# Kernel tuning notes

Measured on AMD Instinct MI355X. Metric: run time of the kernel, lower is better.

Reference implementation:

```python
import jax, jax.numpy as jnp
import numpy as np

B, L = 32, 100
NQ = 500
S = NQ + 1          # n_question + 1 skills
DK, DA, DE = 64, 64, 128
NE, NAT, NIT = 20000, 3000, 3000


def _xavier(k, shape):
    fan_out, fan_in = shape[0], shape[1]
    bound = float(np.sqrt(6.0 / (fan_in + fan_out)))
    return jax.random.uniform(k, shape, jnp.float32, -bound, bound)


def setup_inputs() -> dict:
    key = jax.random.key(0)
    ks = jax.random.split(key, 24)
    inp = {
        'e_data': jax.random.randint(ks[0], (B, L), 0, NE),
        'a_data': jax.random.randint(ks[1], (B, L), 0, 2, dtype=jnp.int32),
        'at_data': jax.random.randint(ks[2], (B, L), 0, NAT),
        'it_data': jax.random.randint(ks[3], (B, L), 0, NIT),
        'q_matrix': (jax.random.uniform(ks[4], (NE + 10, S)) < 0.05).astype(jnp.float32),
        'h0': _xavier(ks[5], (S, DK)),
        'e_embed': _xavier(ks[6], (NE + 10, DE)),
        'at_embed': _xavier(ks[7], (NAT + 10, DK)),
        'it_embed': _xavier(ks[8], (NIT + 10, DK)),
        'W1': _xavier(ks[9], (DK, DA + DE + DK)), 'b1': jnp.zeros((DK,)),
        'W2': _xavier(ks[10], (DK, 4 * DK)),      'b2': jnp.zeros((DK,)),
        'W3': _xavier(ks[11], (DK, 4 * DK)),      'b3': jnp.zeros((DK,)),
        'W4': _xavier(ks[12], (DK, 3 * DK)),      'b4': jnp.zeros((DK,)),
        'W5': _xavier(ks[13], (DK, DE + DK)),     'b5': jnp.zeros((DK,)),
    }
    return inp


def reference(e_data, a_data, at_data, it_data, q_matrix, h0, e_embed,
              at_embed, it_embed, W1, b1, W2, b2, W3, b3, W4, b4, W5, b5):
    b, l = e_data.shape
    dk = h0.shape[1]
    e_emb = e_embed[e_data]            # (B,L,DE)
    it_emb = it_embed[it_data]         # (B,L,DK)
    at_emb = at_embed[at_data]         # (B,L,DK)
    a_rep = jnp.broadcast_to(a_data.astype(jnp.float32)[:, :, None], (b, l, DA))
    # linear_1 over concat(e, at, a): all learning vectors, computed once
    all_learning = jnp.concatenate([e_emb, at_emb, a_rep], axis=2) @ W1.T + b1  # (B,L,DK)

    h_pre0 = jnp.broadcast_to(h0[None], (b,) + h0.shape)      # (B,S,DK)
    h_tilde0 = q_matrix[e_data[:, 0]] @ h0                    # (B,DK)
    learning0 = jnp.zeros((b, dk), jnp.float32)

    xs = dict(
        e_t=e_data[:, :-1].T,                                  # (L-1,B)
        it_t=jnp.swapaxes(it_emb[:, :-1], 0, 1),               # (L-1,B,DK)
        learn_t=jnp.swapaxes(all_learning[:, :-1], 0, 1),      # (L-1,B,DK)
        e_next=e_data[:, 1:].T,                                # (L-1,B)
        e_emb_next=jnp.swapaxes(e_emb[:, 1:], 0, 1),           # (L-1,B,DE)
    )

    def step(carry, x):
        h_pre, h_tilde_pre, learning_pre = carry
        q_e = q_matrix[x['e_t']]                               # (B,S)
        g_in = jnp.concatenate([learning_pre, x['it_t'], x['learn_t'], h_tilde_pre], 1)
        learning_gain = jnp.tanh(g_in @ W2.T + b2)
        gamma_l = jax.nn.sigmoid(g_in @ W3.T + b3)
        LG = gamma_l * (learning_gain + 1.0) * 0.5             # (B,DK)
        LG_tilde = q_e[:, :, None] * LG[:, None, :]            # (B,S,DK)
        s = h_pre.shape[1]
        f_in = jnp.concatenate([
            h_pre,
            jnp.broadcast_to(LG[:, None, :], (b, s, dk)),
            jnp.broadcast_to(x['it_t'][:, None, :], (b, s, dk)),
        ], axis=2)
        gamma_f = jax.nn.sigmoid(f_in @ W4.T + b4)             # (B,S,DK)
        h = LG_tilde + gamma_f * h_pre
        q_next = q_matrix[x['e_next']]                         # (B,S)
        h_tilde = jnp.einsum('bs,bsd->bd', q_next, h)
        y = jax.nn.sigmoid(jnp.concatenate([x['e_emb_next'], h_tilde], 1) @ W5.T + b5).sum(1) / dk
        return (h, h_tilde, x['learn_t']), y

    _, ys = jax.lax.scan(step, (h_pre0, h_tilde0, learning0), xs)
    pred = jnp.concatenate([jnp.zeros((b, 1), jnp.float32), ys.T], axis=1)  # (B,L)
    return pred
```

## Files before the change

kernel.cpp:

```cpp
#include <hip/hip_runtime.h>
#include <hip/hip_bf16.h>

namespace {

constexpr int B  = 32;
constexpr int L  = 100;
constexpr int S  = 501;
constexpr int DK = 64;
constexpr int DE = 128;

typedef __attribute__((ext_vector_type(8))) short short8v;
typedef __attribute__((ext_vector_type(4))) float f32x4;
typedef unsigned int u32;

__device__ __forceinline__ float sigm(float x) {
    return __fdividef(1.0f, 1.0f + __expf(-x));
}
__device__ __forceinline__ unsigned short f2bf(float f) {
    u32 u = __float_as_uint(f);
    u += 0x7FFFu + ((u >> 16) & 1u);
    return (unsigned short)(u >> 16);
}

__global__ __launch_bounds__(256) void k_init(
    const float* __restrict__ W1, const float* __restrict__ W2,
    const float* __restrict__ W3, const float* __restrict__ W4,
    const float* __restrict__ W5,
    float* __restrict__ W1T, float* __restrict__ W2T, float* __restrict__ W3T,
    float* __restrict__ W4T, float* __restrict__ W5T,
    float* __restrict__ pred)
{
    const int idx = blockIdx.x * 256 + threadIdx.x;
    const int st  = gridDim.x * 256;
    for (int i = idx; i < 64 * 256; i += st) {
        int dd = i >> 8, kk = i & 255;
        W1T[kk * 64 + dd] = W1[i];
        W2T[kk * 64 + dd] = W2[i];
        W3T[kk * 64 + dd] = W3[i];
    }
    for (int i = idx; i < 64 * 192; i += st) {
        int dd = i / 192, kk = i % 192;
        W4T[kk * 64 + dd] = W4[i];
        W5T[kk * 64 + dd] = W5[i];
    }
    if (idx < B) pred[idx * L] = 0.0f;
}

__global__ __launch_bounds__(256) void k_all_learning(
    const int* __restrict__ e_data, const int* __restrict__ a_data,
    const int* __restrict__ at_data,
    const float* __restrict__ e_embed, const float* __restrict__ at_embed,
    const float* __restrict__ W1T, const float* __restrict__ b1,
    float* __restrict__ allL)
{
    __shared__ float in_s[4][257];
    const int g = threadIdx.x >> 6;
    const int d = threadIdx.x & 63;
    const int row = blockIdx.x * 4 + g;
    const int e  = e_data[row];
    const int at = at_data[row];
    in_s[g][d]       = e_embed[(size_t)e * DE + d];
    in_s[g][64 + d]  = e_embed[(size_t)e * DE + 64 + d];
    in_s[g][128 + d] = at_embed[(size_t)at * DK + d];
    in_s[g][192 + d] = (float)a_data[row];
    __syncthreads();
    float acc = b1[d];
    #pragma unroll 8
    for (int k = 0; k < 256; ++k) acc += W1T[k * 64 + d] * in_s[g][k];
    allL[row * DK + d] = acc;
}

__global__ __launch_bounds__(256) void k_pre(
    const int* __restrict__ e_data, const int* __restrict__ it_data,
    const float* __restrict__ e_embed, const float* __restrict__ it_embed,
    const float* __restrict__ allL,
    const float* __restrict__ W2T, const float* __restrict__ W3T,
    const float* __restrict__ W4T, const float* __restrict__ W5T,
    const float* __restrict__ b2, const float* __restrict__ b3,
    const float* __restrict__ b4, const float* __restrict__ b5,
    float* __restrict__ G2, float* __restrict__ G3,
    float* __restrict__ G4it, float* __restrict__ prey)
{
    __shared__ float lp[4][64], its[4][64], ln[4][64], ee[4][128];
    const int g = threadIdx.x >> 6;
    const int d = threadIdx.x & 63;
    const int row = blockIdx.x * 4 + g;
    const int t = row % L;
    lp[g][d]  = (t == 0) ? 0.0f : allL[(row - 1) * 64 + d];
    its[g][d] = it_embed[(size_t)it_data[row] * 64 + d];
    ln[g][d]  = allL[row * 64 + d];
    const int e = e_data[row];
    ee[g][d]      = e_embed[(size_t)e * DE + d];
    ee[g][64 + d] = e_embed[(size_t)e * DE + 64 + d];
    __syncthreads();
    float g2 = b2[d], g3 = b3[d], g4 = b4[d], py = b5[d];
    #pragma unroll 4
    for (int k = 0; k < 64; ++k) {
        const float l0 = lp[g][k], i0 = its[g][k], n0 = ln[g][k];
        g2 += W2T[k * 64 + d] * l0 + W2T[(64 + k) * 64 + d] * i0 + W2T[(128 + k) * 64 + d] * n0;
        g3 += W3T[k * 64 + d] * l0 + W3T[(64 + k) * 64 + d] * i0 + W3T[(128 + k) * 64 + d] * n0;
        g4 += W4T[(128 + k) * 64 + d] * i0;
        py += W5T[k * 64 + d] * ee[g][k] + W5T[(64 + k) * 64 + d] * ee[g][64 + k];
    }
    G2[row * 64 + d]   = g2;
    G3[row * 64 + d]   = g3;
    G4it[row * 64 + d] = g4;
    prey[row * 64 + d] = py;
}

__global__ __launch_bounds__(512) void k_steps(
    const float* __restrict__ G2, const float* __restrict__ G3,
    const float* __restrict__ G4it,
    const float* __restrict__ W2, const float* __restrict__ W3,
    const float* __restrict__ W4,
    const float* __restrict__ q_matrix, const int* __restrict__ e_data,
    const float* __restrict__ h0, float* __restrict__ hthist)
{
    __shared__ unsigned short hB[512 * 72];
    __shared__ float qQ[2][512];
    __shared__ float htS[64], LGs[64], Vs[64];
    __shared__ float red[512], red2[512];
    __shared__ int eRow[128];

    const int tid = threadIdx.x;
    const int b   = blockIdx.x;
    const int l   = tid & 63;
    const int w   = tid >> 6;
    const int lm  = l & 15;
    const int lk  = l >> 4;
    const int d   = tid & 63;
    const int kg  = tid >> 6;

    float w2r[8], w3r[8], wbr[8];
    #pragma unroll
    for (int j = 0; j < 8; ++j) {
        w2r[j] = W2[d * 256 + 192 + kg * 8 + j];
        w3r[j] = W3[d * 256 + 192 + kg * 8 + j];
        wbr[j] = W4[d * 192 + 64  + kg * 8 + j];
    }

    short8v afr[4][2];
    #pragma unroll
    for (int dt = 0; dt < 4; ++dt)
        #pragma unroll
        for (int kc = 0; kc < 2; ++kc) {
            const float* src = W4 + (size_t)(dt * 16 + lm) * 192 + kc * 32 + lk * 8;
            union { unsigned short us[8]; short8v v; } u;
            #pragma unroll
            for (int j = 0; j < 8; ++j) u.us[j] = f2bf(src[j]);
            afr[dt][kc] = u.v;
        }

    if (tid < L) eRow[tid] = e_data[b * L + tid];

    f32x4 hreg[4][4];
    #pragma unroll
    for (int st = 0; st < 4; ++st) {
        const int s = (w * 4 + st) * 16 + lm;
        #pragma unroll
        for (int dt = 0; dt < 4; ++dt) {
            const int d0 = dt * 16 + lk * 4;
            f32x4 hv = {0.f, 0.f, 0.f, 0.f};
            if (s < S) hv = *(const f32x4*)(h0 + (size_t)s * 64 + d0);
            hreg[st][dt] = hv;
            const u32 lo = (u32)f2bf(hv.x) | ((u32)f2bf(hv.y) << 16);
            const u32 hi = (u32)f2bf(hv.z) | ((u32)f2bf(hv.w) << 16);
            *(uint2*)&hB[s * 72 + d0] = make_uint2(lo, hi);
        }
    }
    __syncthreads();
    qQ[0][tid] = (tid < S) ? q_matrix[(size_t)eRow[0] * S + tid] : 0.f;
    __syncthreads();

    {
        f32x4 part[4];
        #pragma unroll
        for (int dt = 0; dt < 4; ++dt) part[dt] = f32x4{0.f, 0.f, 0.f, 0.f};
        #pragma unroll
        for (int st = 0; st < 4; ++st) {
            const int s = (w * 4 + st) * 16 + lm;
            const float qe = qQ[0][s];
            #pragma unroll
            for (int dt = 0; dt < 4; ++dt) part[dt] += qe * hreg[st][dt];
        }
        #pragma unroll
        for (int dt = 0; dt < 4; ++dt)
            #pragma unroll
            for (int i = 0; i < 4; ++i) {
                float v = part[dt][i];
                v += __shfl_xor(v, 1); v += __shfl_xor(v, 2);
                v += __shfl_xor(v, 4); v += __shfl_xor(v, 8);
                part[dt][i] = v;
            }
        if (lm == 0) {
            #pragma unroll
            for (int dt = 0; dt < 4; ++dt)
                *(f32x4*)&red[w * 64 + dt * 16 + lk * 4] = part[dt];
        }
        __syncthreads();
        if (tid < 64) {
            float sm = 0.f;
            #pragma unroll
            for (int ww = 0; ww < 8; ++ww) sm += red[ww * 64 + tid];
            htS[tid] = sm;
        }
        __syncthreads();
    }

    for (int t = 0; t < L - 1; ++t) {
        const int cur = t & 1, nxt = cur ^ 1;

        short8v bfr[4][2];
        #pragma unroll
        for (int st = 0; st < 4; ++st) {
            const int s = (w * 4 + st) * 16 + lm;
            #pragma unroll
            for (int kc = 0; kc < 2; ++kc)
                bfr[st][kc] = *(const short8v*)&hB[s * 72 + kc * 32 + lk * 8];
        }

        const float qn = (tid < S) ? q_matrix[(size_t)eRow[t + 1] * S + tid] : 0.f;
        float g2v = 0.f, g3v = 0.f, g4v = 0.f;
        if (tid < 64) {
            g2v = G2[(b * L + t) * 64 + d];
            g3v = G3[(b * L + t) * 64 + d];
            g4v = G4it[(b * L + t) * 64 + d];
        }

        {
            float p2 = 0.f, p3 = 0.f;
            #pragma unroll
            for (int j = 0; j < 8; ++j) {
                const float hv = htS[kg * 8 + j];
                p2 += w2r[j] * hv;
                p3 += w3r[j] * hv;
            }
            red[kg * 64 + d] = p2;
            red2[kg * 64 + d] = p3;
        }
        qQ[nxt][tid] = qn;
        __syncthreads();
        if (tid < 64) {
            float g2 = g2v, g3 = g3v;
            #pragma unroll
            for (int ww = 0; ww < 8; ++ww) { g2 += red[ww * 64 + d]; g3 += red2[ww * 64 + d]; }
            LGs[d] = sigm(g3) * (tanhf(g2) + 1.0f) * 0.5f;
        }
        __syncthreads();
        {
            float pv = 0.f;
            #pragma unroll
            for (int j = 0; j < 8; ++j) pv += wbr[j] * LGs[kg * 8 + j];
            red[kg * 64 + d] = pv;
        }
        __syncthreads();
        if (tid < 64) {
            float v = g4v;
            #pragma unroll
            for (int ww = 0; ww < 8; ++ww) v += red[ww * 64 + d];
            Vs[d] = v;
        }
        __syncthreads();

        f32x4 part[4];
        #pragma unroll
        for (int dt = 0; dt < 4; ++dt) part[dt] = f32x4{0.f, 0.f, 0.f, 0.f};

        #pragma unroll
        for (int half = 0; half < 2; ++half) {
            f32x4 acc[2][4];
            #pragma unroll
            for (int d2 = 0; d2 < 2; ++d2)
                #pragma unroll
                for (int st = 0; st < 4; ++st) acc[d2][st] = f32x4{0.f, 0.f, 0.f, 0.f};

            #pragma unroll
            for (int d2 = 0; d2 < 2; ++d2) {
                const int dt = half * 2 + d2;
                #pragma unroll
                for (int st = 0; st < 4; ++st) {
                    acc[d2][st] = __builtin_amdgcn_mfma_f32_16x16x32_bf16(
                        afr[dt][0], bfr[st][0], acc[d2][st], 0, 0, 0);
                    acc[d2][st] = __builtin_amdgcn_mfma_f32_16x16x32_bf16(
                        afr[dt][1], bfr[st][1], acc[d2][st], 0, 0, 0);
                }
            }

            #pragma unroll
            for (int d2 = 0; d2 < 2; ++d2) {
                const int dt = half * 2 + d2;
                const int d0 = dt * 16 + lk * 4;
                const f32x4 lg4 = *(const f32x4*)&LGs[d0];
                const f32x4 v4  = *(const f32x4*)&Vs[d0];
                #pragma unroll
                for (int st = 0; st < 4; ++st) {
                    const int s = (w * 4 + st) * 16 + lm;
                    const float qe = qQ[cur][s];
                    const float qq = qQ[nxt][s];
                    const f32x4 a  = acc[d2][st];
                    const f32x4 ho = hreg[st][dt];
                    f32x4 hn;
                    hn.x = qe * lg4.x + sigm(a.x + v4.x) * ho.x;
                    hn.y = qe * lg4.y + sigm(a.y + v4.y) * ho.y;
                    hn.z = qe * lg4.z + sigm(a.z + v4.z) * ho.z;
                    hn.w = qe * lg4.w + sigm(a.w + v4.w) * ho.w;
                    hreg[st][dt] = hn;
                    const u32 lo = (u32)f2bf(hn.x) | ((u32)f2bf(hn.y) << 16);
                    const u32 hi = (u32)f2bf(hn.z) | ((u32)f2bf(hn.w) << 16);
                    *(uint2*)&hB[s * 72 + d0] = make_uint2(lo, hi);
                    part[dt] += qq * hn;
                }
            }
        }

        #pragma unroll
        for (int dt = 0; dt < 4; ++dt)
            #pragma unroll
            for (int i = 0; i < 4; ++i) {
                float v = part[dt][i];
                v += __shfl_xor(v, 1); v += __shfl_xor(v, 2);
                v += __shfl_xor(v, 4); v += __shfl_xor(v, 8);
                part[dt][i] = v;
            }
        if (lm == 0) {
            #pragma unroll
            for (int dt = 0; dt < 4; ++dt)
                *(f32x4*)&red[w * 64 + dt * 16 + lk * 4] = part[dt];
        }
        __syncthreads();
        if (tid < 64) {
            float sm = 0.f;
            #pragma unroll
            for (int ww = 0; ww < 8; ++ww) sm += red[ww * 64 + tid];
            htS[tid] = sm;
            hthist[(size_t)(t + 1) * (B * 64) + b * 64 + tid] = sm;
        }
        __syncthreads();
    }
}

__global__ __launch_bounds__(64) void k_y(
    const float* __restrict__ hthist, const float* __restrict__ prey,
    const float* __restrict__ W5T, float* __restrict__ pred)
{
    __shared__ float HT[64];
    const int j = blockIdx.x + 1;
    const int b = blockIdx.y;
    const int d = threadIdx.x;
    HT[d] = hthist[(size_t)j * (B * 64) + b * 64 + d];
    __syncthreads();
    float acc = prey[(b * L + j) * 64 + d];
    #pragma unroll 8
    for (int k = 0; k < 64; ++k) acc += W5T[(128 + k) * 64 + d] * HT[k];
    float y = sigm(acc);
    #pragma unroll
    for (int m = 1; m < 64; m <<= 1) y += __shfl_xor(y, m);
    if (d == 0) pred[b * L + j] = y * (1.0f / 64.0f);
}

}

extern "C" void kernel_launch(void* const* d_in, const int* in_sizes, int n_in,
                              void* d_out, int out_size, void* d_ws, size_t ws_size,
                              hipStream_t stream)
{
    const int*   e_data   = (const int*)d_in[0];
    const int*   a_data   = (const int*)d_in[1];
    const int*   at_data  = (const int*)d_in[2];
    const int*   it_data  = (const int*)d_in[3];
    const float* q_matrix = (const float*)d_in[4];
    const float* h0       = (const float*)d_in[5];
    const float* e_embed  = (const float*)d_in[6];
    const float* at_embed = (const float*)d_in[7];
    const float* it_embed = (const float*)d_in[8];
    const float* W1 = (const float*)d_in[9];  const float* b1 = (const float*)d_in[10];
    const float* W2 = (const float*)d_in[11]; const float* b2 = (const float*)d_in[12];
    const float* W3 = (const float*)d_in[13]; const float* b3 = (const float*)d_in[14];
    const float* W4 = (const float*)d_in[15]; const float* b4 = (const float*)d_in[16];
    const float* W5 = (const float*)d_in[17]; const float* b5 = (const float*)d_in[18];
    float* pred = (float*)d_out;

    float* ws   = (float*)d_ws;
    float* W1T    = ws;
    float* W2T    = W1T    + 16384;
    float* W3T    = W2T    + 16384;
    float* W4T    = W3T    + 16384;
    float* W5T    = W4T    + 12288;
    float* allL   = W5T    + 12288;
    float* G2     = allL   + 204800;
    float* G3     = G2     + 204800;
    float* G4it   = G3     + 204800;
    float* prey   = G4it   + 204800;
    float* hthist = prey   + 204800;

    hipLaunchKernelGGL(k_init, dim3(64), dim3(256), 0, stream,
                       W1, W2, W3, W4, W5, W1T, W2T, W3T, W4T, W5T, pred);
    hipLaunchKernelGGL(k_all_learning, dim3(B * L / 4), dim3(256), 0, stream,
                       e_data, a_data, at_data, e_embed, at_embed, W1T, b1, allL);
    hipLaunchKernelGGL(k_pre, dim3(B * L / 4), dim3(256), 0, stream,
                       e_data, it_data, e_embed, it_embed, allL,
                       W2T, W3T, W4T, W5T, b2, b3, b4, b5, G2, G3, G4it, prey);
    hipLaunchKernelGGL(k_steps, dim3(B), dim3(512), 0, stream,
                       G2, G3, G4it, W2, W3, W4, q_matrix, e_data, h0, hthist);
    hipLaunchKernelGGL(k_y, dim3(L - 1, B), dim3(64), 0, stream,
                       hthist, prey, W5T, pred);
}
```

Before: 798.8 us.

## Collapse per-step gate matvecs into one wave to cut block barriers

The per-step W2/W3/W4 gate matvecs, previously split across all 8 waves with shared-memory reductions and four barriers, are now computed by a single wave. That wave reads weights staged in LDS, which removes three __syncthreads per timestep. The q_matrix row and the G2/G3/G4 values are prefetched one step ahead into registers, and the h_tilde history is buffered in LDS and written to global memory once at the end. In exchange, the matvec work is serialized on 64 threads and LDS use grows to roughly 150KB.

```diff
diff --git a/kernel.cpp b/kernel.cpp
--- a/kernel.cpp
+++ b/kernel.cpp
@@ -108,19 +108,22 @@
     prey[row * 64 + d] = py;
 }
 
-__global__ __launch_bounds__(512) void k_steps(
+__global__ __launch_bounds__(512, 1) void k_steps(
     const float* __restrict__ G2, const float* __restrict__ G3,
     const float* __restrict__ G4it,
-    const float* __restrict__ W2, const float* __restrict__ W3,
-    const float* __restrict__ W4,
+    const float* __restrict__ W2T, const float* __restrict__ W3T,
+    const float* __restrict__ W4T, const float* __restrict__ W4,
     const float* __restrict__ q_matrix, const int* __restrict__ e_data,
     const float* __restrict__ h0, float* __restrict__ hthist)
 {
     __shared__ unsigned short hB[512 * 72];
     __shared__ float qQ[2][512];
-    __shared__ float htS[64], LGs[64], Vs[64];
-    __shared__ float red[512], red2[512];
-    __shared__ int eRow[128];
+    __shared__ float2 w23S[64 * 64];
+    __shared__ float  w4bS[64 * 64];
+    __shared__ float  htH[100 * 64];
+    __shared__ float  LGs[64], Vs[64], htS[64];
+    __shared__ float  red[8 * 64];
+    __shared__ int    eRow[104];
 
     const int tid = threadIdx.x;
     const int b   = blockIdx.x;
@@ -128,16 +131,13 @@
     const int w   = tid >> 6;
     const int lm  = l & 15;
     const int lk  = l >> 4;
-    const int d   = tid & 63;
-    const int kg  = tid >> 6;
-
-    float w2r[8], w3r[8], wbr[8];
-    #pragma unroll
-    for (int j = 0; j < 8; ++j) {
-        w2r[j] = W2[d * 256 + 192 + kg * 8 + j];
-        w3r[j] = W3[d * 256 + 192 + kg * 8 + j];
-        wbr[j] = W4[d * 192 + 64  + kg * 8 + j];
-    }
+
+    for (int i = tid; i < 4096; i += 512) {
+        const int k = i >> 6, dd = i & 63;
+        w23S[i] = make_float2(W2T[(192 + k) * 64 + dd], W3T[(192 + k) * 64 + dd]);
+        w4bS[i] = W4T[(64 + k) * 64 + dd];
+    }
+    if (tid < L) eRow[tid] = e_data[b * L + tid];
 
     short8v afr[4][2];
     #pragma unroll
@@ -150,8 +150,6 @@
             for (int j = 0; j < 8; ++j) u.us[j] = f2bf(src[j]);
             afr[dt][kc] = u.v;
         }
-
-    if (tid < L) eRow[tid] = e_data[b * L + tid];
 
     f32x4 hreg[4][4];
     #pragma unroll
@@ -169,7 +167,19 @@
         }
     }
     __syncthreads();
-    qQ[0][tid] = (tid < S) ? q_matrix[(size_t)eRow[0] * S + tid] : 0.f;
+
+    float qn_reg;
+    {
+        const float q0 = (tid < S) ? q_matrix[(size_t)eRow[0] * S + tid] : 0.f;
+        qQ[0][tid] = q0;
+        qn_reg = (tid < S) ? q_matrix[(size_t)eRow[1] * S + tid] : 0.f;
+    }
+    float g2v = 0.f, g3v = 0.f, g4v = 0.f;
+    if (tid < 64) {
+        g2v = G2[(b * L) * 64 + l];
+        g3v = G3[(b * L) * 64 + l];
+        g4v = G4it[(b * L) * 64 + l];
+    }
     __syncthreads();
 
     {
@@ -197,19 +207,17 @@
             for (int dt = 0; dt < 4; ++dt)
                 *(f32x4*)&red[w * 64 + dt * 16 + lk * 4] = part[dt];
         }
-        __syncthreads();
-        if (tid < 64) {
-            float sm = 0.f;
-            #pragma unroll
-            for (int ww = 0; ww < 8; ++ww) sm += red[ww * 64 + tid];
-            htS[tid] = sm;
-        }
-        __syncthreads();
-    }
+    }
+    __syncthreads();
 
     for (int t = 0; t < L - 1; ++t) {
         const int cur = t & 1, nxt = cur ^ 1;
 
+        qQ[nxt][tid] = qn_reg;
+        {
+            const int tn = (t + 2 < L) ? t + 2 : L - 1;
+            qn_reg = (tid < S) ? q_matrix[(size_t)eRow[tn] * S + tid] : 0.f;
+        }
         short8v bfr[4][2];
         #pragma unroll
         for (int st = 0; st < 4; ++st) {
@@ -219,46 +227,39 @@
                 bfr[st][kc] = *(const short8v*)&hB[s * 72 + kc * 32 + lk * 8];
         }
 
-        const float qn = (tid < S) ? q_matrix[(size_t)eRow[t + 1] * S + tid] : 0.f;
-        float g2v = 0.f, g3v = 0.f, g4v = 0.f;
         if (tid < 64) {
-            g2v = G2[(b * L + t) * 64 + d];
-            g3v = G3[(b * L + t) * 64 + d];
-            g4v = G4it[(b * L + t) * 64 + d];
-        }
-
-        {
-            float p2 = 0.f, p3 = 0.f;
-            #pragma unroll
-            for (int j = 0; j < 8; ++j) {
-                const float hv = htS[kg * 8 + j];
-                p2 += w2r[j] * hv;
-                p3 += w3r[j] * hv;
-            }
-            red[kg * 64 + d] = p2;
-            red2[kg * 64 + d] = p3;
-        }
-        qQ[nxt][tid] = qn;
-        __syncthreads();
-        if (tid < 64) {
-            float g2 = g2v, g3 = g3v;
-            #pragma unroll
-            for (int ww = 0; ww < 8; ++ww) { g2 += red[ww * 64 + d]; g3 += red2[ww * 64 + d]; }
-            LGs[d] = sigm(g3) * (tanhf(g2) + 1.0f) * 0.5f;
-        }
-        __syncthreads();
-        {
-            float pv = 0.f;
-            #pragma unroll
-            for (int j = 0; j < 8; ++j) pv += wbr[j] * LGs[kg * 8 + j];
-            red[kg * 64 + d] = pv;
-        }
-        __syncthreads();
-        if (tid < 64) {
-            float v = g4v;
-            #pragma unroll
-            for (int ww = 0; ww < 8; ++ww) v += red[ww * 64 + d];
-            Vs[d] = v;
+            const float g2c = g2v, g3c = g3v, g4c = g4v;
+            g2v = G2[(b * L + t + 1) * 64 + l];
+            g3v = G3[(b * L + t + 1) * 64 + l];
+            g4v = G4it[(b * L + t + 1) * 64 + l];
+
+            float htd = 0.f;
+            #pragma unroll
+            for (int ww = 0; ww < 8; ++ww) htd += red[ww * 64 + l];
+            htS[l] = htd;
+            htH[t * 64 + l] = htd;
+
+            float g2 = g2c, g3 = g3c;
+            #pragma unroll
+            for (int k4 = 0; k4 < 16; ++k4) {
+                const f32x4 h4 = *(const f32x4*)&htS[k4 * 4];
+                #pragma unroll
+                for (int j = 0; j < 4; ++j) {
+                    const float2 wv = w23S[(k4 * 4 + j) * 64 + l];
+                    g2 += wv.x * h4[j];
+                    g3 += wv.y * h4[j];
+                }
+            }
+            const float lg = sigm(g3) * (tanhf(g2) + 1.0f) * 0.5f;
+            LGs[l] = lg;
+            float v = g4c;
+            #pragma unroll
+            for (int k4 = 0; k4 < 16; ++k4) {
+                const f32x4 lg4 = *(const f32x4*)&LGs[k4 * 4];
+                #pragma unroll
+                for (int j = 0; j < 4; ++j) v += w4bS[(k4 * 4 + j) * 64 + l] * lg4[j];
+            }
+            Vs[l] = v;
         }
         __syncthreads();
 
@@ -328,15 +329,17 @@
                 *(f32x4*)&red[w * 64 + dt * 16 + lk * 4] = part[dt];
         }
         __syncthreads();
-        if (tid < 64) {
-            float sm = 0.f;
-            #pragma unroll
-            for (int ww = 0; ww < 8; ++ww) sm += red[ww * 64 + tid];
-            htS[tid] = sm;
-            hthist[(size_t)(t + 1) * (B * 64) + b * 64 + tid] = sm;
-        }
-        __syncthreads();
-    }
+    }
+
+    if (tid < 64) {
+        float htd = 0.f;
+        #pragma unroll
+        for (int ww = 0; ww < 8; ++ww) htd += red[ww * 64 + l];
+        htH[99 * 64 + l] = htd;
+    }
+    __syncthreads();
+    for (int i = tid; i < 100 * 64; i += 512)
+        hthist[(size_t)(i >> 6) * (B * 64) + b * 64 + (i & 63)] = htH[i];
 }
 
 __global__ __launch_bounds__(64) void k_y(
@@ -401,7 +404,8 @@
                        e_data, it_data, e_embed, it_embed, allL,
                        W2T, W3T, W4T, W5T, b2, b3, b4, b5, G2, G3, G4it, prey);
     hipLaunchKernelGGL(k_steps, dim3(B), dim3(512), 0, stream,
-                       G2, G3, G4it, W2, W3, W4, q_matrix, e_data, h0, hthist);
+                       G2, G3, G4it, W2T, W3T, W4T, W4,
+                       q_matrix, e_data, h0, hthist);
     hipLaunchKernelGGL(k_y, dim3(L - 1, B), dim3(64), 0, stream,
                        hthist, prey, W5T, pred);
 }
```

Result: slower. 1.360 ms (+70.3%).

## Prefetch q rows and G inputs a step ahead and shorten ht reductions

Applied to the files above, without the earlier changes.

The recurrent step kernel now loads the q_matrix row two steps ahead into a register and packs the current and next q values into one float2 shared array. It also loads next-step G2/G3/G4 values early, so global latency is hidden behind the current step. The h_tilde reduction uses two shuffle stages plus a 32-way shared-memory sum instead of four shuffles, and the h_tilde history is staged in LDS and written out once at the end. This raises LDS use (about 25KB more) and sets launch bounds to one block per SM.

```diff
diff --git a/kernel.cpp b/kernel.cpp
--- a/kernel.cpp
+++ b/kernel.cpp
@@ -20,6 +20,9 @@
     u32 u = __float_as_uint(f);
     u += 0x7FFFu + ((u >> 16) & 1u);
     return (unsigned short)(u >> 16);
+}
+__device__ __forceinline__ u32 pack2(float a, float b) {
+    return (u32)f2bf(a) | ((u32)f2bf(b) << 16);
 }
 
 __global__ __launch_bounds__(256) void k_init(
@@ -108,7 +111,7 @@
     prey[row * 64 + d] = py;
 }
 
-__global__ __launch_bounds__(512) void k_steps(
+__global__ __launch_bounds__(512, 1) void k_steps(
     const float* __restrict__ G2, const float* __restrict__ G3,
     const float* __restrict__ G4it,
     const float* __restrict__ W2, const float* __restrict__ W3,
@@ -117,10 +120,12 @@
     const float* __restrict__ h0, float* __restrict__ hthist)
 {
     __shared__ unsigned short hB[512 * 72];
-    __shared__ float qQ[2][512];
+    __shared__ float2 qP[512];
+    __shared__ float htH[100 * 64];
     __shared__ float htS[64], LGs[64], Vs[64];
     __shared__ float red[512], red2[512];
-    __shared__ int eRow[128];
+    __shared__ float red4[32 * 64];
+    __shared__ int eRow[104];
 
     const int tid = threadIdx.x;
     const int b   = blockIdx.x;
@@ -163,13 +168,23 @@
             f32x4 hv = {0.f, 0.f, 0.f, 0.f};
             if (s < S) hv = *(const f32x4*)(h0 + (size_t)s * 64 + d0);
             hreg[st][dt] = hv;
-            const u32 lo = (u32)f2bf(hv.x) | ((u32)f2bf(hv.y) << 16);
-            const u32 hi = (u32)f2bf(hv.z) | ((u32)f2bf(hv.w) << 16);
-            *(uint2*)&hB[s * 72 + d0] = make_uint2(lo, hi);
-        }
-    }
-    __syncthreads();
-    qQ[0][tid] = (tid < S) ? q_matrix[(size_t)eRow[0] * S + tid] : 0.f;
+            *(uint2*)&hB[s * 72 + d0] =
+                make_uint2(pack2(hv.x, hv.y), pack2(hv.z, hv.w));
+        }
+    }
+    __syncthreads();
+
+    {
+        const float q0 = (tid < S) ? q_matrix[(size_t)eRow[0] * S + tid] : 0.f;
+        const float q1 = (tid < S) ? q_matrix[(size_t)eRow[1] * S + tid] : 0.f;
+        qP[tid] = make_float2(q0, q1);
+    }
+    float g2v = 0.f, g3v = 0.f, g4v = 0.f;
+    if (tid < 64) {
+        g2v = G2[(b * L) * 64 + l];
+        g3v = G3[(b * L) * 64 + l];
+        g4v = G4it[(b * L) * 64 + l];
+    }
     __syncthreads();
 
     {
@@ -179,7 +194,7 @@
         #pragma unroll
         for (int st = 0; st < 4; ++st) {
             const int s = (w * 4 + st) * 16 + lm;
-            const float qe = qQ[0][s];
+            const float qe = qP[s].x;
             #pragma unroll
             for (int dt = 0; dt < 4; ++dt) part[dt] += qe * hreg[st][dt];
         }
@@ -189,27 +204,36 @@
             for (int i = 0; i < 4; ++i) {
                 float v = part[dt][i];
                 v += __shfl_xor(v, 1); v += __shfl_xor(v, 2);
-                v += __shfl_xor(v, 4); v += __shfl_xor(v, 8);
                 part[dt][i] = v;
             }
-        if (lm == 0) {
+        if ((lm & 3) == 0) {
+            const int g = w * 4 + (lm >> 2);
             #pragma unroll
             for (int dt = 0; dt < 4; ++dt)
-                *(f32x4*)&red[w * 64 + dt * 16 + lk * 4] = part[dt];
-        }
-        __syncthreads();
-        if (tid < 64) {
-            float sm = 0.f;
-            #pragma unroll
-            for (int ww = 0; ww < 8; ++ww) sm += red[ww * 64 + tid];
-            htS[tid] = sm;
-        }
-        __syncthreads();
-    }
+                *(f32x4*)&red4[g * 64 + dt * 16 + lk * 4] = part[dt];
+        }
+    }
+    __syncthreads();
+    if (tid < 64) {
+        float htd = 0.f;
+        #pragma unroll
+        for (int g = 0; g < 32; ++g) htd += red4[g * 64 + l];
+        htS[l] = htd;
+        htH[l] = htd;
+    }
+    __syncthreads();
+
+    float qn_reg = 0.f;
 
     for (int t = 0; t < L - 1; ++t) {
-        const int cur = t & 1, nxt = cur ^ 1;
-
+        if (t > 0) {
+            const float2 qold = qP[tid];
+            qP[tid] = make_float2(qold.y, qn_reg);
+        }
+        {
+            const int tn = (t + 2 < L) ? t + 2 : L - 1;
+            qn_reg = (tid < S) ? q_matrix[(size_t)eRow[tn] * S + tid] : 0.f;
+        }
         short8v bfr[4][2];
         #pragma unroll
         for (int st = 0; st < 4; ++st) {
@@ -218,28 +242,20 @@
             for (int kc = 0; kc < 2; ++kc)
                 bfr[st][kc] = *(const short8v*)&hB[s * 72 + kc * 32 + lk * 8];
         }
-
-        const float qn = (tid < S) ? q_matrix[(size_t)eRow[t + 1] * S + tid] : 0.f;
-        float g2v = 0.f, g3v = 0.f, g4v = 0.f;
-        if (tid < 64) {
-            g2v = G2[(b * L + t) * 64 + d];
-            g3v = G3[(b * L + t) * 64 + d];
-            g4v = G4it[(b * L + t) * 64 + d];
-        }
-
         {
+            const f32x4 h4a = *(const f32x4*)&htS[kg * 8];
+            const f32x4 h4b = *(const f32x4*)&htS[kg * 8 + 4];
             float p2 = 0.f, p3 = 0.f;
             #pragma unroll
-            for (int j = 0; j < 8; ++j) {
-                const float hv = htS[kg * 8 + j];
-                p2 += w2r[j] * hv;
-                p3 += w3r[j] * hv;
+            for (int j = 0; j < 4; ++j) {
+                p2 += w2r[j] * h4a[j] + w2r[4 + j] * h4b[j];
+                p3 += w3r[j] * h4a[j] + w3r[4 + j] * h4b[j];
             }
-            red[kg * 64 + d] = p2;
+            red[kg * 64 + d]  = p2;
             red2[kg * 64 + d] = p3;
         }
-        qQ[nxt][tid] = qn;
-        __syncthreads();
+        __syncthreads();
+
         if (tid < 64) {
             float g2 = g2v, g3 = g3v;
             #pragma unroll
@@ -247,20 +263,32 @@
             LGs[d] = sigm(g3) * (tanhf(g2) + 1.0f) * 0.5f;
         }
         __syncthreads();
+
         {
+            const f32x4 l4a = *(const f32x4*)&LGs[kg * 8];
+            const f32x4 l4b = *(const f32x4*)&LGs[kg * 8 + 4];
             float pv = 0.f;
             #pragma unroll
-            for (int j = 0; j < 8; ++j) pv += wbr[j] * LGs[kg * 8 + j];
+            for (int j = 0; j < 4; ++j)
+                pv += wbr[j] * l4a[j] + wbr[4 + j] * l4b[j];
             red[kg * 64 + d] = pv;
         }
         __syncthreads();
+
         if (tid < 64) {
             float v = g4v;
             #pragma unroll
             for (int ww = 0; ww < 8; ++ww) v += red[ww * 64 + d];
             Vs[d] = v;
-        }
-        __syncthreads();
+            g2v = G2[(b * L + t + 1) * 64 + l];
+            g3v = G3[(b * L + t + 1) * 64 + l];
+            g4v = G4it[(b * L + t + 1) * 64 + l];
+        }
+        __syncthreads();
+
+        float2 qv[4];
+        #pragma unroll
+        for (int st = 0; st < 4; ++st) qv[st] = qP[(w * 4 + st) * 16 + lm];
 
         f32x4 part[4];
         #pragma unroll
@@ -295,8 +323,8 @@
                 #pragma unroll
                 for (int st = 0; st < 4; ++st) {
                     const int s = (w * 4 + st) * 16 + lm;
-                    const float qe = qQ[cur][s];
-                    const float qq = qQ[nxt][s];
+                    const float qe = qv[st].x;
+                    const float qq = qv[st].y;
                     const f32x4 a  = acc[d2][st];
                     const f32x4 ho = hreg[st][dt];
                     f32x4 hn;
@@ -305,9 +333,8 @@
                     hn.z = qe * lg4.z + sigm(a.z + v4.z) * ho.z;
                     hn.w = qe * lg4.w + sigm(a.w + v4.w) * ho.w;
                     hreg[st][dt] = hn;
-                    const u32 lo = (u32)f2bf(hn.x) | ((u32)f2bf(hn.y) << 16);
-                    const u32 hi = (u32)f2bf(hn.z) | ((u32)f2bf(hn.w) << 16);
-                    *(uint2*)&hB[s * 72 + d0] = make_uint2(lo, hi);
+                    *(uint2*)&hB[s * 72 + d0] =
+                        make_uint2(pack2(hn.x, hn.y), pack2(hn.z, hn.w));
                     part[dt] += qq * hn;
                 }
             }
@@ -319,24 +346,28 @@
             for (int i = 0; i < 4; ++i) {
                 float v = part[dt][i];
                 v += __shfl_xor(v, 1); v += __shfl_xor(v, 2);
-                v += __shfl_xor(v, 4); v += __shfl_xor(v, 8);
                 part[dt][i] = v;
             }
-        if (lm == 0) {
+        if ((lm & 3) == 0) {
+            const int g = w * 4 + (lm >> 2);
             #pragma unroll
             for (int dt = 0; dt < 4; ++dt)
-                *(f32x4*)&red[w * 64 + dt * 16 + lk * 4] = part[dt];
-        }
-        __syncthreads();
+                *(f32x4*)&red4[g * 64 + dt * 16 + lk * 4] = part[dt];
+        }
+        __syncthreads();
+
         if (tid < 64) {
-            float sm = 0.f;
-            #pragma unroll
-            for (int ww = 0; ww < 8; ++ww) sm += red[ww * 64 + tid];
-            htS[tid] = sm;
-            hthist[(size_t)(t + 1) * (B * 64) + b * 64 + tid] = sm;
-        }
-        __syncthreads();
-    }
+            float htd = 0.f;
+            #pragma unroll
+            for (int g = 0; g < 32; ++g) htd += red4[g * 64 + l];
+            htS[l] = htd;
+            htH[(t + 1) * 64 + l] = htd;
+        }
+        __syncthreads();
+    }
+
+    for (int i = tid; i < 100 * 64; i += 512)
+        hthist[(size_t)(i >> 6) * (B * 64) + b * 64 + (i & 63)] = htH[i];
 }
 
 __global__ __launch_bounds__(64) void k_y(
```

Measured after the change: 755.1 us. 5.5% less time.
